# Performance work log

Hardware: AMD Instinct MI355X
Metric: run time of the kernel (lower is better)

Reference implementation:

```python
import jax, jax.numpy as jnp
import numpy as np

N_QUBITS = 12
MAX_LAYERS = 21
Q_DEPTH = 20
DIM = 2 ** N_QUBITS  # 4096
Q_DELTA = 0.01


def setup_inputs() -> dict:
    key = jax.random.key(0)
    k1, k2 = jax.random.split(key)
    return {
        "input_features": jax.random.normal(k1, (4096, 2048), dtype=jnp.float32),
        "q_params": Q_DELTA * jax.random.normal(k2, (MAX_LAYERS * N_QUBITS,), dtype=jnp.float32),
    }


def _cnot(state, c, t):
    # state: (B, 2,2,...,2); flip target axis where control bit == 1
    s0, s1 = jnp.split(state, 2, axis=c + 1)
    s1 = jnp.flip(s1, axis=t + 1)
    return jnp.concatenate([s0, s1], axis=c + 1)


def _ry(state, theta, w):
    # real RY rotation: [[cos(t/2), -sin(t/2)], [sin(t/2), cos(t/2)]]
    s0, s1 = jnp.split(state, 2, axis=w + 1)
    c = jnp.cos(theta * 0.5)
    s = jnp.sin(theta * 0.5)
    return jnp.concatenate([c * s0 - s * s1, s * s0 + c * s1], axis=w + 1)


def _entangling_layer(state):
    for i in range(0, N_QUBITS - 1, 2):
        state = _cnot(state, i, i + 1)
    for i in range(1, N_QUBITS - 1, 2):
        state = _cnot(state, i, i + 1)
    return state


def _forward(input_features, q_params):
    q_in = jnp.tanh(input_features) * (np.pi / 2.0)
    B, F = q_in.shape
    # AmplitudeEmbedding: pad with 0.5 to 2^n, then L2-normalize
    padded = jnp.concatenate(
        [q_in, jnp.full((B, DIM - F), 0.5, dtype=q_in.dtype)], axis=1
    )
    state = padded / jnp.linalg.norm(padded, axis=1, keepdims=True)
    state = state.reshape((B,) + (2,) * N_QUBITS)  # qubit 0 = most significant axis

    weights = q_params.reshape(MAX_LAYERS, N_QUBITS)

    @jax.checkpoint
    def layer(st, theta):
        st = _entangling_layer(st)
        for j in range(N_QUBITS):
            st = _ry(st, theta[j], j)
        return st, None

    state, _ = jax.lax.scan(layer, state, weights[1:1 + Q_DEPTH])

    probs = jnp.square(state.reshape(B, DIM))  # (B, 4096)
    bit_pos = N_QUBITS - 1 - jnp.arange(N_QUBITS)
    bits = (jnp.arange(DIM)[:, None] >> bit_pos[None, :]) & 1  # (DIM, 12)
    signs = (1.0 - 2.0 * bits).astype(probs.dtype)
    return probs @ signs  # (B, 12) expvals of PauliZ per qubit


def reference(input_features, q_params):
    return _forward(input_features, q_params)
```

## Files before the change

### kernel.cpp

```cpp
#include <hip/hip_runtime.h>
#include <math.h>

#define LAYERS 20
#define CS_FLOATS 480

__global__ void cs_precompute(const float* __restrict__ qp, float* __restrict__ cs) {
    int i = threadIdx.x;
    if (i < 240) {
        float t = 0.5f * qp[12 + i];
        cs[2 * i]     = cosf(t);
        cs[2 * i + 1] = sinf(t);
    }
}

#define ALL32(F) F(0) F(1) F(2) F(3) F(4) F(5) F(6) F(7) F(8) F(9) F(10) F(11) \
  F(12) F(13) F(14) F(15) F(16) F(17) F(18) F(19) F(20) F(21) F(22) F(23) \
  F(24) F(25) F(26) F(27) F(28) F(29) F(30) F(31)

#define P16(F) F(0,16) F(1,17) F(2,18) F(3,19) F(4,20) F(5,21) F(6,22) F(7,23) \
  F(8,24) F(9,25) F(10,26) F(11,27) F(12,28) F(13,29) F(14,30) F(15,31)
#define P8(F) F(0,8) F(1,9) F(2,10) F(3,11) F(4,12) F(5,13) F(6,14) F(7,15) \
  F(16,24) F(17,25) F(18,26) F(19,27) F(20,28) F(21,29) F(22,30) F(23,31)
#define P4(F) F(0,4) F(1,5) F(2,6) F(3,7) F(8,12) F(9,13) F(10,14) F(11,15) \
  F(16,20) F(17,21) F(18,22) F(19,23) F(24,28) F(25,29) F(26,30) F(27,31)
#define P2(F) F(0,2) F(1,3) F(4,6) F(5,7) F(8,10) F(9,11) F(12,14) F(13,15) \
  F(16,18) F(17,19) F(20,22) F(21,23) F(24,26) F(25,27) F(28,30) F(29,31)
#define P1(F) F(0,1) F(2,3) F(4,5) F(6,7) F(8,9) F(10,11) F(12,13) F(14,15) \
  F(16,17) F(18,19) F(20,21) F(22,23) F(24,25) F(26,27) F(28,29) F(30,31)

#define XA(F) F(0,0,1) F(1,2,3) F(2,4,5) F(3,6,7) F(4,8,9) F(5,10,11) F(6,12,13) F(7,14,15)
#define XB(F) F(0,16,17) F(1,18,19) F(2,20,21) F(3,22,23) F(4,24,25) F(5,26,27) F(6,28,29) F(7,30,31)

template <int CTRL>
__device__ __forceinline__ float dppf(float x) {
    return __int_as_float(__builtin_amdgcn_mov_dpp(
        __float_as_int(x), CTRL, 0xF, 0xF, true));
}

template <bool PRE>
__global__ __launch_bounds__(128)
void qsim(const float* __restrict__ feats,
          const float* __restrict__ qp,
          const float* __restrict__ cs,
          float* __restrict__ out)
{
    __shared__ float2 xch2[2 * 64 * 9];
    float* xchf = (float*)xch2;

    const int tid  = threadIdx.x;
    const int lane = tid & 63;
    const int w    = tid >> 6;
    const int row  = blockIdx.x;

    const int sl0   = lane ^ (lane >> 1) ^ ((lane >> 2) & 5);
    const int addr0 = sl0 << 2;
    const int addr1 = (sl0 ^ 48) << 2;

    const int mybase = w * 576 + lane * 9;
    const int pbase  = (1 - w) * 576 + lane * 9;

#define DCL(r) float v##r;
    ALL32(DCL)
#undef DCL

    const float* fr = feats + (size_t)row * 2048;
    if (w == 0) {
        float fsum = 0.f;
#define LD(r) { float x_ = tanhf(fr[((r) << 6) + lane]) * 1.5707963267948966f; \
                v##r = x_; fsum += x_ * x_; }
        ALL32(LD)
#undef LD
#pragma unroll
        for (int m = 32; m >= 1; m >>= 1) fsum += __shfl_xor(fsum, m, 64);
        if (lane == 0) xchf[0] = fsum;
    }
    __syncthreads();
    const float inv = rsqrtf(xchf[0] + 512.0f);
    __syncthreads();
    if (w == 0) {
#define SC(r) v##r *= inv;
        ALL32(SC)
#undef SC
    } else {
        const float padv = 0.5f * inv;
#define PD(r) v##r = padv;
        ALL32(PD)
#undef PD
    }

#pragma unroll 1
    for (int l = 0; l < LAYERS; ++l) {
        const float* csl = cs + l * 24;

#define BPV(a, x) __int_as_float(__builtin_amdgcn_ds_bpermute( \
                      (((a) & 1) ? addr1 : addr0), __float_as_int(x)))
#define FIX(a) v##a = BPV(a, v##a);
#define C2(a,b) { float t_ = v##a; v##a = BPV(a, v##b); v##b = BPV(b, t_); }
#define C4(a,b,c,d) { float t_ = v##a; v##a = BPV(a, v##b); \
        v##b = BPV(b, v##c); v##c = BPV(c, v##d); v##d = BPV(d, t_); }
#define C8(a,b,c,d,e,f,g,h) { float t_ = v##a; v##a = BPV(a, v##b); \
        v##b = BPV(b, v##c); v##c = BPV(c, v##d); v##d = BPV(d, v##e); \
        v##e = BPV(e, v##f); v##f = BPV(f, v##g); v##g = BPV(g, v##h); \
        v##h = BPV(h, t_); }
        if (w == 0) {
            FIX(0) FIX(1)
            C2(2, 3)
            C4(4, 7, 5, 6)
            C4(8, 12, 11, 14)
            C4(9, 13, 10, 15)
            C8(16, 28, 23, 25, 17, 29, 22, 24)
            C8(18, 31, 21, 26, 19, 30, 20, 27)
        } else {
            C8(0, 16, 12, 27, 2, 19, 14, 24)
            C8(1, 17, 13, 26, 3, 18, 15, 25)
            C8(4, 23, 9, 29, 6, 20, 11, 30)
            C8(5, 22, 8, 28, 7, 21, 10, 31)
        }
#undef BPV
#undef FIX
#undef C2
#undef C4
#undef C8

#define RYP(a,b) { float a0_ = v##a, a1_ = v##b; \
        v##a = c_ * a0_ - s_ * a1_; v##b = s_ * a0_ + c_ * a1_; }
#define RYREG(J, LIST) { float c_, s_; \
        if constexpr (PRE) { c_ = csl[2*(J)]; s_ = csl[2*(J)+1]; } \
        else { float t_ = 0.5f * qp[12 + l*12 + (J)]; __sincosf(t_, &s_, &c_); } \
        LIST(RYP) }
        RYREG(1, P16)
        RYREG(2, P8)
        RYREG(3, P4)
        RYREG(4, P2)
        RYREG(5, P1)
#undef RYREG
#undef RYP

        {
            float c_, s_, ssel_;
#define GETCS(jj) \
            if constexpr (PRE) { c_ = csl[12 + 2*(jj)]; s_ = csl[13 + 2*(jj)]; } \
            else { float t_ = 0.5f * qp[12 + l*12 + 6 + (jj)]; __sincosf(t_, &s_, &c_); }

            GETCS(0); ssel_ = (lane & 32) ? s_ : -s_;
#define LRYS(r) { float p_ = __shfl_xor(v##r, 32, 64); v##r = c_ * v##r + ssel_ * p_; }
            ALL32(LRYS)
#undef LRYS
            GETCS(1); ssel_ = (lane & 16) ? s_ : -s_;
#define LRYS(r) { float p_ = __shfl_xor(v##r, 16, 64); v##r = c_ * v##r + ssel_ * p_; }
            ALL32(LRYS)
#undef LRYS
            GETCS(2); ssel_ = (lane & 8) ? s_ : -s_;
#define LRYS(r) { float hi_ = dppf<0x118>(v##r), lo_ = dppf<0x108>(v##r); \
                  float p_ = (lane & 8) ? lo_ : hi_; v##r = c_ * v##r + ssel_ * p_; }
            ALL32(LRYS)
#undef LRYS
            GETCS(3); ssel_ = (lane & 4) ? s_ : -s_;
#define LRYS(r) { float hi_ = dppf<0x114>(v##r), lo_ = dppf<0x104>(v##r); \
                  float p_ = (lane & 4) ? lo_ : hi_; v##r = c_ * v##r + ssel_ * p_; }
            ALL32(LRYS)
#undef LRYS
            GETCS(4); ssel_ = (lane & 2) ? s_ : -s_;
#define LRYS(r) { float p_ = dppf<0x4E>(v##r); v##r = c_ * v##r + ssel_ * p_; }
            ALL32(LRYS)
#undef LRYS
            GETCS(5); ssel_ = (lane & 1) ? s_ : -s_;
#define LRYS(r) { float p_ = dppf<0xB1>(v##r); v##r = c_ * v##r + ssel_ * p_; }
            ALL32(LRYS)
#undef LRYS
#undef GETCS
        }

        {
            float c0_, s0_;
            if constexpr (PRE) { c0_ = csl[0]; s0_ = csl[1]; }
            else { float t_ = 0.5f * qp[12 + l*12]; __sincosf(t_, &s0_, &c0_); }
            const float ssel0_ = w ? s0_ : -s0_;
#define XW(k,a,b) xch2[mybase + (k)] = make_float2(v##a, v##b);
#define XR(k,a,b) { float2 p_ = xch2[pbase + (k)]; \
        v##a = c0_ * v##a + ssel0_ * p_.x; \
        v##b = c0_ * v##b + ssel0_ * p_.y; }
            XA(XW)
            __syncthreads();
            XA(XR)
            __syncthreads();
            XB(XW)
            __syncthreads();
            XB(XR)
            __syncthreads();
#undef XW
#undef XR
        }
    }

    float T = 0.f;
#define SQT(r) v##r *= v##r; T += v##r;
    ALL32(SQT)
#undef SQT

    float part[12];
    part[0] = w ? -T : T;
#define ADDB(a,b) + v##b
    { float S;
      S = 0.f P16(ADDB); part[1] = T - 2.f * S;
      S = 0.f P8(ADDB);  part[2] = T - 2.f * S;
      S = 0.f P4(ADDB);  part[3] = T - 2.f * S;
      S = 0.f P2(ADDB);  part[4] = T - 2.f * S;
      S = 0.f P1(ADDB);  part[5] = T - 2.f * S; }
#undef ADDB
#pragma unroll
    for (int q = 6; q < 12; ++q) {
        const int m = 32 >> (q - 6);
        part[q] = (lane & m) ? -T : T;
    }
#pragma unroll
    for (int q = 0; q < 12; ++q) {
#pragma unroll
        for (int m2 = 32; m2 >= 1; m2 >>= 1) part[q] += __shfl_xor(part[q], m2, 64);
    }
    if (lane == 0) {
#pragma unroll
        for (int q = 0; q < 12; ++q) xchf[w * 12 + q] = part[q];
    }
    __syncthreads();
    if (tid < 12) out[row * 12 + tid] = xchf[tid] + xchf[12 + tid];
}

extern "C" void kernel_launch(void* const* d_in, const int* in_sizes, int n_in,
                              void* d_out, int out_size, void* d_ws, size_t ws_size,
                              hipStream_t stream) {
    (void)in_sizes; (void)n_in; (void)out_size;
    const float* feats = (const float*)d_in[0];
    const float* qp    = (const float*)d_in[1];
    float* out = (float*)d_out;

    if (ws_size >= CS_FLOATS * sizeof(float)) {
        float* cs = (float*)d_ws;
        cs_precompute<<<1, 256, 0, stream>>>(qp, cs);
        qsim<true><<<4096, 128, 0, stream>>>(feats, qp, cs, out);
    } else {
        qsim<false><<<4096, 128, 0, stream>>>(feats, qp, nullptr, out);
    }
}
```

Baseline: 390.4 us.

## Pack state into float2 vectors for packed FMA and cheaper lane exchanges

Stores the 32 per-lane amplitudes as 16 float2 vectors so the rotation arithmetic can map onto packed FP32 instructions (v_pk_fma). The qubit-5 rotation becomes an in-register swap of the pair's halves. The lane exchanges also change: the xor-32 shuffle becomes a direct ds_bpermute, xor-16 and xor-4 use ds_swizzle, and the xor-8 case uses a single row_ror DPP in place of two DPP moves plus a select. Packing may add register-pairing moves, and swizzle goes through the LDS pipe where DPP did not.

Result: faster. 316.9 us (-18.8%).

```diff
diff --git a/kernel.cpp b/kernel.cpp
--- a/kernel.cpp
+++ b/kernel.cpp
@@ -3,6 +3,8 @@
 
 #define LAYERS 20
 #define CS_FLOATS 480
+
+typedef float f2 __attribute__((ext_vector_type(2)));
 
 __global__ void cs_precompute(const float* __restrict__ qp, float* __restrict__ cs) {
     int i = threadIdx.x;
@@ -13,9 +15,49 @@
     }
 }
 
-#define ALL32(F) F(0) F(1) F(2) F(3) F(4) F(5) F(6) F(7) F(8) F(9) F(10) F(11) \
+#define S0 u0.x
+#define S1 u0.y
+#define S2 u1.x
+#define S3 u1.y
+#define S4 u2.x
+#define S5 u2.y
+#define S6 u3.x
+#define S7 u3.y
+#define S8 u4.x
+#define S9 u4.y
+#define S10 u5.x
+#define S11 u5.y
+#define S12 u6.x
+#define S13 u6.y
+#define S14 u7.x
+#define S15 u7.y
+#define S16 u8.x
+#define S17 u8.y
+#define S18 u9.x
+#define S19 u9.y
+#define S20 u10.x
+#define S21 u10.y
+#define S22 u11.x
+#define S23 u11.y
+#define S24 u12.x
+#define S25 u12.y
+#define S26 u13.x
+#define S27 u13.y
+#define S28 u14.x
+#define S29 u14.y
+#define S30 u15.x
+#define S31 u15.y
+
+#define ALL16(F) F(0) F(1) F(2) F(3) F(4) F(5) F(6) F(7) F(8) F(9) F(10) F(11) \
+  F(12) F(13) F(14) F(15)
+#define ALL32S(F) F(0) F(1) F(2) F(3) F(4) F(5) F(6) F(7) F(8) F(9) F(10) F(11) \
   F(12) F(13) F(14) F(15) F(16) F(17) F(18) F(19) F(20) F(21) F(22) F(23) \
   F(24) F(25) F(26) F(27) F(28) F(29) F(30) F(31)
+
+#define KQ1(F) F(0,8) F(1,9) F(2,10) F(3,11) F(4,12) F(5,13) F(6,14) F(7,15)
+#define KQ2(F) F(0,4) F(1,5) F(2,6) F(3,7) F(8,12) F(9,13) F(10,14) F(11,15)
+#define KQ3(F) F(0,2) F(1,3) F(4,6) F(5,7) F(8,10) F(9,11) F(12,14) F(13,15)
+#define KQ4(F) F(0,1) F(2,3) F(4,5) F(6,7) F(8,9) F(10,11) F(12,13) F(14,15)
 
 #define P16(F) F(0,16) F(1,17) F(2,18) F(3,19) F(4,20) F(5,21) F(6,22) F(7,23) \
   F(8,24) F(9,25) F(10,26) F(11,27) F(12,28) F(13,29) F(14,30) F(15,31)
@@ -28,13 +70,17 @@
 #define P1(F) F(0,1) F(2,3) F(4,5) F(6,7) F(8,9) F(10,11) F(12,13) F(14,15) \
   F(16,17) F(18,19) F(20,21) F(22,23) F(24,25) F(26,27) F(28,29) F(30,31)
 
-#define XA(F) F(0,0,1) F(1,2,3) F(2,4,5) F(3,6,7) F(4,8,9) F(5,10,11) F(6,12,13) F(7,14,15)
-#define XB(F) F(0,16,17) F(1,18,19) F(2,20,21) F(3,22,23) F(4,24,25) F(5,26,27) F(6,28,29) F(7,30,31)
+#define XA16(F) F(0) F(1) F(2) F(3) F(4) F(5) F(6) F(7)
+#define XB16(F) F(8) F(9) F(10) F(11) F(12) F(13) F(14) F(15)
 
 template <int CTRL>
 __device__ __forceinline__ float dppf(float x) {
     return __int_as_float(__builtin_amdgcn_mov_dpp(
         __float_as_int(x), CTRL, 0xF, 0xF, true));
+}
+template <int IMM>
+__device__ __forceinline__ float swzf(float x) {
+    return __int_as_float(__builtin_amdgcn_ds_swizzle(__float_as_int(x), IMM));
 }
 
 template <bool PRE>
@@ -44,7 +90,7 @@
           const float* __restrict__ cs,
           float* __restrict__ out)
 {
-    __shared__ float2 xch2[2 * 64 * 9];
+    __shared__ f2 xch2[2 * 64 * 9];
     float* xchf = (float*)xch2;
 
     const int tid  = threadIdx.x;
@@ -52,23 +98,24 @@
     const int w    = tid >> 6;
     const int row  = blockIdx.x;
 
-    const int sl0   = lane ^ (lane >> 1) ^ ((lane >> 2) & 5);
-    const int addr0 = sl0 << 2;
-    const int addr1 = (sl0 ^ 48) << 2;
+    const int sl0     = lane ^ (lane >> 1) ^ ((lane >> 2) & 5);
+    const int addr0   = sl0 << 2;
+    const int addr1   = (sl0 ^ 48) << 2;
+    const int addrX32 = (lane ^ 32) << 2;
 
     const int mybase = w * 576 + lane * 9;
     const int pbase  = (1 - w) * 576 + lane * 9;
 
-#define DCL(r) float v##r;
-    ALL32(DCL)
-#undef DCL
+#define DCLU(k) f2 u##k;
+    ALL16(DCLU)
+#undef DCLU
 
     const float* fr = feats + (size_t)row * 2048;
     if (w == 0) {
         float fsum = 0.f;
 #define LD(r) { float x_ = tanhf(fr[((r) << 6) + lane]) * 1.5707963267948966f; \
-                v##r = x_; fsum += x_ * x_; }
-        ALL32(LD)
+                S##r = x_; fsum += x_ * x_; }
+        ALL32S(LD)
 #undef LD
 #pragma unroll
         for (int m = 32; m >= 1; m >>= 1) fsum += __shfl_xor(fsum, m, 64);
@@ -78,13 +125,14 @@
     const float inv = rsqrtf(xchf[0] + 512.0f);
     __syncthreads();
     if (w == 0) {
-#define SC(r) v##r *= inv;
-        ALL32(SC)
+#define SC(k) u##k *= inv;
+        ALL16(SC)
 #undef SC
     } else {
         const float padv = 0.5f * inv;
-#define PD(r) v##r = padv;
-        ALL32(PD)
+        const f2 pv2 = {padv, padv};
+#define PD(k) u##k = pv2;
+        ALL16(PD)
 #undef PD
     }
 
@@ -94,14 +142,14 @@
 
 #define BPV(a, x) __int_as_float(__builtin_amdgcn_ds_bpermute( \
                       (((a) & 1) ? addr1 : addr0), __float_as_int(x)))
-#define FIX(a) v##a = BPV(a, v##a);
-#define C2(a,b) { float t_ = v##a; v##a = BPV(a, v##b); v##b = BPV(b, t_); }
-#define C4(a,b,c,d) { float t_ = v##a; v##a = BPV(a, v##b); \
-        v##b = BPV(b, v##c); v##c = BPV(c, v##d); v##d = BPV(d, t_); }
-#define C8(a,b,c,d,e,f,g,h) { float t_ = v##a; v##a = BPV(a, v##b); \
-        v##b = BPV(b, v##c); v##c = BPV(c, v##d); v##d = BPV(d, v##e); \
-        v##e = BPV(e, v##f); v##f = BPV(f, v##g); v##g = BPV(g, v##h); \
-        v##h = BPV(h, t_); }
+#define FIX(a) S##a = BPV(a, S##a);
+#define C2(a,b) { float t_ = S##a; S##a = BPV(a, S##b); S##b = BPV(b, t_); }
+#define C4(a,b,c,d) { float t_ = S##a; S##a = BPV(a, S##b); \
+        S##b = BPV(b, S##c); S##c = BPV(c, S##d); S##d = BPV(d, t_); }
+#define C8(a,b,c,d,e,f,g,h) { float t_ = S##a; S##a = BPV(a, S##b); \
+        S##b = BPV(b, S##c); S##c = BPV(c, S##d); S##d = BPV(d, S##e); \
+        S##e = BPV(e, S##f); S##f = BPV(f, S##g); S##g = BPV(g, S##h); \
+        S##h = BPV(h, t_); }
         if (w == 0) {
             FIX(0) FIX(1)
             C2(2, 3)
@@ -122,52 +170,64 @@
 #undef C4
 #undef C8
 
-#define RYP(a,b) { float a0_ = v##a, a1_ = v##b; \
-        v##a = c_ * a0_ - s_ * a1_; v##b = s_ * a0_ + c_ * a1_; }
-#define RYREG(J, LIST) { float c_, s_; \
+#define RYPK(a,b) { f2 A_ = u##a, B_ = u##b; \
+        u##a = c_ * A_ - s_ * B_; u##b = s_ * A_ + c_ * B_; }
+#define RYREGK(J, LIST) { float c_, s_; \
         if constexpr (PRE) { c_ = csl[2*(J)]; s_ = csl[2*(J)+1]; } \
         else { float t_ = 0.5f * qp[12 + l*12 + (J)]; __sincosf(t_, &s_, &c_); } \
-        LIST(RYP) }
-        RYREG(1, P16)
-        RYREG(2, P8)
-        RYREG(3, P4)
-        RYREG(4, P2)
-        RYREG(5, P1)
-#undef RYREG
-#undef RYP
+        LIST(RYPK) }
+        RYREGK(1, KQ1)
+        RYREGK(2, KQ2)
+        RYREGK(3, KQ3)
+        RYREGK(4, KQ4)
+#undef RYREGK
+#undef RYPK
+
+        {
+            float c_, s_;
+            if constexpr (PRE) { c_ = csl[10]; s_ = csl[11]; }
+            else { float t_ = 0.5f * qp[12 + l*12 + 5]; __sincosf(t_, &s_, &c_); }
+            const f2 ss5_ = {-s_, s_};
+#define Q5(k) { f2 sw_ = u##k.yx; u##k = c_ * u##k + ss5_ * sw_; }
+            ALL16(Q5)
+#undef Q5
+        }
 
         {
             float c_, s_, ssel_;
 #define GETCS(jj) \
             if constexpr (PRE) { c_ = csl[12 + 2*(jj)]; s_ = csl[13 + 2*(jj)]; } \
             else { float t_ = 0.5f * qp[12 + l*12 + 6 + (jj)]; __sincosf(t_, &s_, &c_); }
+#define LQ(k, EX) { f2 p_; p_.x = EX(u##k.x); p_.y = EX(u##k.y); \
+                    u##k = c_ * u##k + ssel_ * p_; }
 
             GETCS(0); ssel_ = (lane & 32) ? s_ : -s_;
-#define LRYS(r) { float p_ = __shfl_xor(v##r, 32, 64); v##r = c_ * v##r + ssel_ * p_; }
-            ALL32(LRYS)
-#undef LRYS
+#define EX6(x) __int_as_float(__builtin_amdgcn_ds_bpermute(addrX32, __float_as_int(x)))
+#define LQ6(k) LQ(k, EX6)
+            ALL16(LQ6)
+#undef LQ6
+#undef EX6
             GETCS(1); ssel_ = (lane & 16) ? s_ : -s_;
-#define LRYS(r) { float p_ = __shfl_xor(v##r, 16, 64); v##r = c_ * v##r + ssel_ * p_; }
-            ALL32(LRYS)
-#undef LRYS
+#define LQ7(k) LQ(k, swzf<0x401F>)
+            ALL16(LQ7)
+#undef LQ7
             GETCS(2); ssel_ = (lane & 8) ? s_ : -s_;
-#define LRYS(r) { float hi_ = dppf<0x118>(v##r), lo_ = dppf<0x108>(v##r); \
-                  float p_ = (lane & 8) ? lo_ : hi_; v##r = c_ * v##r + ssel_ * p_; }
-            ALL32(LRYS)
-#undef LRYS
+#define LQ8(k) LQ(k, dppf<0x128>)
+            ALL16(LQ8)
+#undef LQ8
             GETCS(3); ssel_ = (lane & 4) ? s_ : -s_;
-#define LRYS(r) { float hi_ = dppf<0x114>(v##r), lo_ = dppf<0x104>(v##r); \
-                  float p_ = (lane & 4) ? lo_ : hi_; v##r = c_ * v##r + ssel_ * p_; }
-            ALL32(LRYS)
-#undef LRYS
+#define LQ9(k) LQ(k, swzf<0x101F>)
+            ALL16(LQ9)
+#undef LQ9
             GETCS(4); ssel_ = (lane & 2) ? s_ : -s_;
-#define LRYS(r) { float p_ = dppf<0x4E>(v##r); v##r = c_ * v##r + ssel_ * p_; }
-            ALL32(LRYS)
-#undef LRYS
+#define LQ10(k) LQ(k, dppf<0x4E>)
+            ALL16(LQ10)
+#undef LQ10
             GETCS(5); ssel_ = (lane & 1) ? s_ : -s_;
-#define LRYS(r) { float p_ = dppf<0xB1>(v##r); v##r = c_ * v##r + ssel_ * p_; }
-            ALL32(LRYS)
-#undef LRYS
+#define LQ11(k) LQ(k, dppf<0xB1>)
+            ALL16(LQ11)
+#undef LQ11
+#undef LQ
 #undef GETCS
         }
 
@@ -176,31 +236,33 @@
             if constexpr (PRE) { c0_ = csl[0]; s0_ = csl[1]; }
             else { float t_ = 0.5f * qp[12 + l*12]; __sincosf(t_, &s0_, &c0_); }
             const float ssel0_ = w ? s0_ : -s0_;
-#define XW(k,a,b) xch2[mybase + (k)] = make_float2(v##a, v##b);
-#define XR(k,a,b) { float2 p_ = xch2[pbase + (k)]; \
-        v##a = c0_ * v##a + ssel0_ * p_.x; \
-        v##b = c0_ * v##b + ssel0_ * p_.y; }
-            XA(XW)
+#define XWA(k) xch2[mybase + (k)] = u##k;
+#define XRA(k) { f2 p_ = xch2[pbase + (k)]; u##k = c0_ * u##k + ssel0_ * p_; }
+#define XWB(k) xch2[mybase + ((k) - 8)] = u##k;
+#define XRB(k) { f2 p_ = xch2[pbase + ((k) - 8)]; u##k = c0_ * u##k + ssel0_ * p_; }
+            XA16(XWA)
             __syncthreads();
-            XA(XR)
+            XA16(XRA)
             __syncthreads();
-            XB(XW)
+            XB16(XWB)
             __syncthreads();
-            XB(XR)
+            XB16(XRB)
             __syncthreads();
-#undef XW
-#undef XR
+#undef XWA
+#undef XRA
+#undef XWB
+#undef XRB
         }
     }
 
     float T = 0.f;
-#define SQT(r) v##r *= v##r; T += v##r;
-    ALL32(SQT)
+#define SQT(k) u##k *= u##k; T += u##k.x + u##k.y;
+    ALL16(SQT)
 #undef SQT
 
     float part[12];
     part[0] = w ? -T : T;
-#define ADDB(a,b) + v##b
+#define ADDB(a,b) + S##b
     { float S;
       S = 0.f P16(ADDB); part[1] = T - 2.f * S;
       S = 0.f P8(ADDB);  part[2] = T - 2.f * S;
```
